# Performance work log

Hardware: AMD Instinct MI355X
Metric: run time of the kernel (lower is better)

The kernel has to match this reference:

```python
import jax, jax.numpy as jnp
import numpy as np

TH = 0.95      # hardcoded entropy threshold in the 'normal' branch of forward
EPS = 1e-12    # eps added to distances in get_entropy

B, C, K, D = 262144, 1000, 3, 64  # batch, num_classes, num_centers, feature_dim


def setup_inputs() -> dict:
    key = jax.random.key(0)
    k1, k2, k3 = jax.random.split(key, 3)
    x = jax.random.normal(k1, (B, D), dtype=jnp.float32)
    labels = jax.random.randint(k2, (B,), 0, C, dtype=jnp.int32)
    centers = jax.random.normal(k3, (C, K, D), dtype=jnp.float32)  # nn.Parameter, init_way='normal'
    return {"x": x, "labels": labels, "centers": centers}


def reference(x, labels, centers):
    # The torch code builds the full [B, C, K] distance tensor and then gathers the
    # label's class; only the positive-class distances are ever used, so we gather
    # the centers first (same math, no [B, C, K, D] / [B, C, K] blowup).
    c = centers[labels]                                   # [B, K, D]
    pos = jnp.sum((x[:, None, :] - c) ** 2, axis=-1)      # [B, K] squared distances

    min_pos = jnp.min(pos, axis=1)                        # [B]

    # two smallest distances, ascending (== sorted_values[:2])
    two_smallest = -jax.lax.top_k(-pos, 2)[0]             # [B, 2]
    d = two_smallest + EPS
    p = d[:, 0] / (d[:, 0] + d[:, 1])                     # p <= 0.5
    entropy = -(p * jnp.log2(p) + (1.0 - p) * jnp.log2(1.0 - p))
    mask = entropy <= TH                                  # mask[i]=False when entropy > 0.95 (num_centers>1)

    loss1 = jnp.mean(min_pos)
    cnt = jnp.sum(mask.astype(min_pos.dtype))
    loss2 = jnp.sum(jnp.where(mask, min_pos, 0.0)) / cnt  # == min_pos[mask].mean()
    return loss1, loss2
```

## Files before the change

kernel.cpp:

```cpp
#include <hip/hip_runtime.h>


#define TH   0.95f
#define EPSF 1e-12f
#define NBLK 2048
#define BLK  256

__global__ __launch_bounds__(BLK, 8) void mp_main(
    const float* __restrict__ x,
    const int*   __restrict__ labels,
    const float* __restrict__ centers,
    float*       __restrict__ partials,
    int B)
{
    const int tid  = threadIdx.x;
    const int lane = tid & 63;
    const int wave = tid >> 6;
    const int sub  = lane & 15;
    const int rsub = lane >> 4;

    const float4* __restrict__ x4 = (const float4*)x;
    const float4* __restrict__ c4 = (const float4*)centers;

    const int rows_per_block = B / NBLK;
    const int iters = rows_per_block / 16;
    const int row0 = blockIdx.x * rows_per_block;

    float s1 = 0.f, s2 = 0.f, sc = 0.f;

    for (int t = 0; t < iters; ++t) {
        const int row = row0 + t * 16 + wave * 4 + rsub;

        const float4 xv = x4[row * 16 + sub];
        const int lab = labels[row];

        const float4* cb = c4 + lab * 48 + sub;
        float a0, a1, a2;
        {
            float4 cv = cb[0];
            float dx = xv.x - cv.x, dy = xv.y - cv.y, dz = xv.z - cv.z, dw = xv.w - cv.w;
            a0 = dx * dx + dy * dy + dz * dz + dw * dw;
        }
        {
            float4 cv = cb[16];
            float dx = xv.x - cv.x, dy = xv.y - cv.y, dz = xv.z - cv.z, dw = xv.w - cv.w;
            a1 = dx * dx + dy * dy + dz * dz + dw * dw;
        }
        {
            float4 cv = cb[32];
            float dx = xv.x - cv.x, dy = xv.y - cv.y, dz = xv.z - cv.z, dw = xv.w - cv.w;
            a2 = dx * dx + dy * dy + dz * dz + dw * dw;
        }

        #pragma unroll
        for (int m = 1; m <= 8; m <<= 1) {
            a0 += __shfl_xor(a0, m);
            a1 += __shfl_xor(a1, m);
            a2 += __shfl_xor(a2, m);
        }

        const float mn  = fminf(a0, fminf(a1, a2));
        const float mx  = fmaxf(a0, fmaxf(a1, a2));
        const float mid = a0 + a1 + a2 - mn - mx;

        const float d0 = mn + EPSF, d1 = mid + EPSF;
        const float p  = d0 / (d0 + d1);
        const float q  = 1.f - p;
        const float ent = -(p * __log2f(p) + q * __log2f(q));
        const float msk = (ent <= TH) ? 1.f : 0.f;

        const float w = (sub == 0) ? 1.f : 0.f;
        s1 += w * mn;
        s2 += w * msk * mn;
        sc += w * msk;
    }

    #pragma unroll
    for (int m = 1; m <= 32; m <<= 1) {
        s1 += __shfl_xor(s1, m);
        s2 += __shfl_xor(s2, m);
        sc += __shfl_xor(sc, m);
    }

    __shared__ float red[3][4];
    if (lane == 0) { red[0][wave] = s1; red[1][wave] = s2; red[2][wave] = sc; }
    __syncthreads();
    if (tid == 0) {
        partials[blockIdx.x]              = red[0][0] + red[0][1] + red[0][2] + red[0][3];
        partials[NBLK + blockIdx.x]       = red[1][0] + red[1][1] + red[1][2] + red[1][3];
        partials[2 * NBLK + blockIdx.x]   = red[2][0] + red[2][1] + red[2][2] + red[2][3];
    }
}

__global__ __launch_bounds__(BLK) void mp_final(
    const float* __restrict__ partials, float* __restrict__ out, float invB)
{
    const int tid  = threadIdx.x;
    const int lane = tid & 63;
    const int wave = tid >> 6;

    float s1 = 0.f, s2 = 0.f, sc = 0.f;
    for (int i = tid; i < NBLK; i += BLK) {
        s1 += partials[i];
        s2 += partials[NBLK + i];
        sc += partials[2 * NBLK + i];
    }
    #pragma unroll
    for (int m = 1; m <= 32; m <<= 1) {
        s1 += __shfl_xor(s1, m);
        s2 += __shfl_xor(s2, m);
        sc += __shfl_xor(sc, m);
    }
    __shared__ float red[3][4];
    if (lane == 0) { red[0][wave] = s1; red[1][wave] = s2; red[2][wave] = sc; }
    __syncthreads();
    if (tid == 0) {
        float t1 = red[0][0] + red[0][1] + red[0][2] + red[0][3];
        float t2 = red[1][0] + red[1][1] + red[1][2] + red[1][3];
        float t3 = red[2][0] + red[2][1] + red[2][2] + red[2][3];
        out[0] = t1 * invB;
        out[1] = t2 / t3;
    }
}

extern "C" void kernel_launch(void* const* d_in, const int* in_sizes, int n_in,
                              void* d_out, int out_size, void* d_ws, size_t ws_size,
                              hipStream_t stream) {
    const float* x       = (const float*)d_in[0];
    const int*   labels  = (const int*)d_in[1];
    const float* centers = (const float*)d_in[2];
    float* out      = (float*)d_out;
    float* partials = (float*)d_ws;
    const int B = in_sizes[1];

    mp_main<<<NBLK, BLK, 0, stream>>>(x, labels, centers, partials, B);
    mp_final<<<1, BLK, 0, stream>>>(partials, out, 1.0f / (float)B);
}
```

Baseline: 107.8 us.

## Map each row to 4 lanes with 4 float4 loads to cut shuffle reductions

Changes the thread-to-row mapping so each row is handled by 4 lanes instead of 16, with every lane loading four strided float4s of x and of each center. This cuts the cross-lane shuffle reduction from 4 rounds to 2 per distance, gives each thread more independent loads in flight, and uses FMA accumulation. Launch bounds change from 8 to 4 waves per SIMD to leave room for the extra registers, which may reduce occupancy. Each row's loads stay 256B-contiguous across its 4 lanes (stride-4 float4 pattern), so coalescing per row is kept.

```diff
diff --git a/kernel.cpp b/kernel.cpp
--- a/kernel.cpp
+++ b/kernel.cpp
@@ -6,7 +6,33 @@
 #define NBLK 2048
 #define BLK  256
 
-__global__ __launch_bounds__(BLK, 8) void mp_main(
+__device__ __forceinline__ float dist16(const float4 xv0, const float4 xv1,
+                                        const float4 xv2, const float4 xv3,
+                                        const float4* __restrict__ cb) {
+    const float4 c0 = cb[0];
+    const float4 c1 = cb[4];
+    const float4 c2 = cb[8];
+    const float4 c3 = cb[12];
+    float d = xv0.x - c0.x; float s = d * d;
+    d = xv0.y - c0.y; s = fmaf(d, d, s);
+    d = xv0.z - c0.z; s = fmaf(d, d, s);
+    d = xv0.w - c0.w; s = fmaf(d, d, s);
+    d = xv1.x - c1.x; s = fmaf(d, d, s);
+    d = xv1.y - c1.y; s = fmaf(d, d, s);
+    d = xv1.z - c1.z; s = fmaf(d, d, s);
+    d = xv1.w - c1.w; s = fmaf(d, d, s);
+    d = xv2.x - c2.x; s = fmaf(d, d, s);
+    d = xv2.y - c2.y; s = fmaf(d, d, s);
+    d = xv2.z - c2.z; s = fmaf(d, d, s);
+    d = xv2.w - c2.w; s = fmaf(d, d, s);
+    d = xv3.x - c3.x; s = fmaf(d, d, s);
+    d = xv3.y - c3.y; s = fmaf(d, d, s);
+    d = xv3.z - c3.z; s = fmaf(d, d, s);
+    d = xv3.w - c3.w; s = fmaf(d, d, s);
+    return s;
+}
+
+__global__ __launch_bounds__(BLK, 4) void mp_main(
     const float* __restrict__ x,
     const int*   __restrict__ labels,
     const float* __restrict__ centers,
@@ -16,48 +42,36 @@
     const int tid  = threadIdx.x;
     const int lane = tid & 63;
     const int wave = tid >> 6;
-    const int sub  = lane & 15;
-    const int rsub = lane >> 4;
+    const int sub  = lane & 3;
+    const int r    = lane >> 2;
 
     const float4* __restrict__ x4 = (const float4*)x;
     const float4* __restrict__ c4 = (const float4*)centers;
 
     const int rows_per_block = B / NBLK;
-    const int iters = rows_per_block / 16;
-    const int row0 = blockIdx.x * rows_per_block;
+    const int iters = rows_per_block >> 6;
+    const int rbase = blockIdx.x * rows_per_block + wave * 16 + r;
 
     float s1 = 0.f, s2 = 0.f, sc = 0.f;
 
     for (int t = 0; t < iters; ++t) {
-        const int row = row0 + t * 16 + wave * 4 + rsub;
+        const int row = rbase + (t << 6);
 
-        const float4 xv = x4[row * 16 + sub];
+        const float4* xr = x4 + row * 16 + sub;
+        const float4 xv0 = xr[0];
+        const float4 xv1 = xr[4];
+        const float4 xv2 = xr[8];
+        const float4 xv3 = xr[12];
+
         const int lab = labels[row];
+        const float4* cb = c4 + lab * 48 + sub;
 
-        const float4* cb = c4 + lab * 48 + sub;
-        float a0, a1, a2;
-        {
-            float4 cv = cb[0];
-            float dx = xv.x - cv.x, dy = xv.y - cv.y, dz = xv.z - cv.z, dw = xv.w - cv.w;
-            a0 = dx * dx + dy * dy + dz * dz + dw * dw;
-        }
-        {
-            float4 cv = cb[16];
-            float dx = xv.x - cv.x, dy = xv.y - cv.y, dz = xv.z - cv.z, dw = xv.w - cv.w;
-            a1 = dx * dx + dy * dy + dz * dz + dw * dw;
-        }
-        {
-            float4 cv = cb[32];
-            float dx = xv.x - cv.x, dy = xv.y - cv.y, dz = xv.z - cv.z, dw = xv.w - cv.w;
-            a2 = dx * dx + dy * dy + dz * dz + dw * dw;
-        }
+        float a0 = dist16(xv0, xv1, xv2, xv3, cb);
+        float a1 = dist16(xv0, xv1, xv2, xv3, cb + 16);
+        float a2 = dist16(xv0, xv1, xv2, xv3, cb + 32);
 
-        #pragma unroll
-        for (int m = 1; m <= 8; m <<= 1) {
-            a0 += __shfl_xor(a0, m);
-            a1 += __shfl_xor(a1, m);
-            a2 += __shfl_xor(a2, m);
-        }
+        a0 += __shfl_xor(a0, 1); a1 += __shfl_xor(a1, 1); a2 += __shfl_xor(a2, 1);
+        a0 += __shfl_xor(a0, 2); a1 += __shfl_xor(a1, 2); a2 += __shfl_xor(a2, 2);
 
         const float mn  = fminf(a0, fminf(a1, a2));
         const float mx  = fmaxf(a0, fmaxf(a1, a2));
```

Measured after the change: 103.1 us. -4.4%, faster.
